# Kernel optimization log

Measured on AMD Instinct MI355X. Metric: run time of the kernel, lower is better.

The kernel has to match this reference:

```python
import jax, jax.numpy as jnp
import numpy as np

CROP = 48
THRESHOLD = 0.5
IOU_THRESHOLD = 0.5


def _conv(x, w, b):
    # x: [N,H,W,C], w: [kh,kw,Cin,Cout]
    y = jax.lax.conv_general_dilated(x, w, (1, 1), 'VALID',
                                     dimension_numbers=('NHWC', 'HWIO', 'NHWC'))
    return y + b


def _prelu(x, a):
    # a broadcasts over the channel-last axis
    return jnp.where(x >= 0, x, a * x)


def _maxpool(x, k, s, p):
    return jax.lax.reduce_window(x, -jnp.inf, jax.lax.max,
                                 (1, k, k, 1), (1, s, s, 1),
                                 ((0, 0), (p, p), (p, p), (0, 0)))


def _nms_keep(boxes, scores, valid, iou_thr):
    # fixed-shape greedy NMS (torchvision semantics: suppress iou > thr)
    N = boxes.shape[0]
    s = jnp.where(valid, scores, -jnp.inf)
    order = jnp.argsort(-s)
    b = boxes[order]
    x1, y1, x2, y2 = b[:, 0], b[:, 1], b[:, 2], b[:, 3]
    area = (x2 - x1) * (y2 - y1)
    xx1 = jnp.maximum(x1[:, None], x1[None, :])
    yy1 = jnp.maximum(y1[:, None], y1[None, :])
    xx2 = jnp.minimum(x2[:, None], x2[None, :])
    yy2 = jnp.minimum(y2[:, None], y2[None, :])
    inter = jnp.clip(xx2 - xx1, 0.0) * jnp.clip(yy2 - yy1, 0.0)
    iou = inter / (area[:, None] + area[None, :] - inter + 1e-12)
    keep0 = valid[order]
    idx = jnp.arange(N)

    def body(i, keep):
        sup = (iou[i] > iou_thr) & (idx > i) & keep[i] & keep
        return keep & ~sup

    keep_sorted = jax.lax.fori_loop(0, N, body, keep0)
    return jnp.zeros(N, bool).at[order].set(keep_sorted)


def setup_inputs() -> dict:
    key = jax.random.key(0)
    ks = jax.random.split(key, 24)
    H = W = 1024
    N = 2048
    image = jax.random.uniform(ks[0], (H, W, 3), jnp.float32) * 255.0
    x1 = jax.random.uniform(ks[1], (N,), jnp.float32) * (W - 130)
    y1 = jax.random.uniform(ks[2], (N,), jnp.float32) * (H - 130)
    bw = 20.0 + jax.random.uniform(ks[3], (N,), jnp.float32) * 100.0
    bh = 20.0 + jax.random.uniform(ks[4], (N,), jnp.float32) * 100.0
    bboxes = jnp.stack([x1, y1, x1 + bw, y1 + bh], axis=1)
    rn = lambda k, sh, s: jax.random.normal(k, sh, jnp.float32) * s
    return {
        'bboxes': bboxes, 'image': image,
        'conv1_w': rn(ks[5], (3, 3, 3, 32), 0.05), 'conv1_b': rn(ks[6], (32,), 0.01),
        'prelu1': 0.25 * jnp.ones((32,), jnp.float32),
        'conv2_w': rn(ks[7], (3, 3, 32, 64), 0.05), 'conv2_b': rn(ks[8], (64,), 0.01),
        'prelu2': 0.25 * jnp.ones((64,), jnp.float32),
        'conv3_w': rn(ks[9], (3, 3, 64, 64), 0.05), 'conv3_b': rn(ks[10], (64,), 0.01),
        'prelu3': 0.25 * jnp.ones((64,), jnp.float32),
        'conv4_w': rn(ks[11], (2, 2, 64, 128), 0.05), 'conv4_b': rn(ks[12], (128,), 0.01),
        'prelu4': 0.25 * jnp.ones((128,), jnp.float32),
        'fc5_w': rn(ks[13], (256, 1152), 0.02), 'fc5_b': rn(ks[14], (256,), 0.01),
        'prelu5': 0.25 * jnp.ones((256,), jnp.float32),
        'fc6a_w': rn(ks[15], (2, 256), 0.1), 'fc6a_b': rn(ks[16], (2,), 0.01),
        'fc6b_w': rn(ks[17], (4, 256), 0.1), 'fc6b_b': rn(ks[18], (4,), 0.01),
    }


def reference(bboxes, image, conv1_w, conv1_b, prelu1, conv2_w, conv2_b, prelu2,
              conv3_w, conv3_b, prelu3, conv4_w, conv4_b, prelu4,
              fc5_w, fc5_b, prelu5, fc6a_w, fc6a_b, fc6b_w, fc6b_b):
    H, W = image.shape[0], image.shape[1]
    N = bboxes.shape[0]
    # preprocess (torch: (x - 127.5) * 0.0078125)
    data = (image - 127.5) * 0.0078125  # [H,W,3]
    # clip boxes in place like the torch forward
    bx1 = jnp.clip(bboxes[:, 0], 0.0, None)
    by1 = jnp.clip(bboxes[:, 1], 0.0, None)
    bx2 = jnp.clip(bboxes[:, 2], None, float(W))
    by2 = jnp.clip(bboxes[:, 3], None, float(H))
    bb = jnp.stack([bx1, by1, bx2, by2], axis=1)  # clipped boxes [N,4]
    # integer crop windows (torch .int() truncation; coords >= 0)
    ib = bb.astype(jnp.int32)
    cw = jnp.maximum(ib[:, 2] - ib[:, 0], 1)
    ch = jnp.maximum(ib[:, 3] - ib[:, 1], 1)
    # nearest-neighbor resize to 48x48 (F.interpolate default mode='nearest')
    r = jnp.arange(CROP, dtype=jnp.int32)
    xs = ib[:, 0:1] + (r[None, :] * cw[:, None]) // CROP  # [N,48]
    ys = ib[:, 1:2] + (r[None, :] * ch[:, None]) // CROP  # [N,48]
    crops = data[ys[:, :, None], xs[:, None, :], :]  # [N,48,48,3] gather
    # CNN trunk
    h = _maxpool(_prelu(_conv(crops, conv1_w, conv1_b), prelu1), 3, 2, 1)
    h = _maxpool(_prelu(_conv(h, conv2_w, conv2_b), prelu2), 3, 2, 0)
    h = _maxpool(_prelu(_conv(h, conv3_w, conv3_b), prelu3), 2, 2, 0)
    h = _prelu(_conv(h, conv4_w, conv4_b), prelu4)  # [N,3,3,128]
    h = jnp.transpose(h, (0, 3, 1, 2)).reshape(N, -1)  # NCHW flatten like torch -> [N,1152]
    h = _prelu(h @ fc5_w.T + fc5_b, prelu5)  # [N,256]
    cls = jax.nn.softmax(h @ fc6a_w.T + fc6a_b, axis=1)  # [N,2]
    reg = h @ fc6b_w.T + fc6b_b  # [N,4]
    score = cls[:, 1]
    valid = score >= THRESHOLD
    w = bb[:, 2] - bb[:, 0]
    hgt = bb[:, 3] - bb[:, 1]
    out = jnp.stack([bb[:, 0] + reg[:, 0] * w,
                     bb[:, 1] + reg[:, 1] * hgt,
                     bb[:, 2] + reg[:, 2] * w,
                     bb[:, 3] + reg[:, 3] * hgt], axis=1)  # [N,4]
    keep = _nms_keep(out, score, valid, IOU_THRESHOLD)
    return jnp.where(keep[:, None], out, 0.0)
```

## Files before the change

kernel.cpp:

```cpp
#include <hip/hip_runtime.h>
#include <math.h>
#include <stdint.h>

#define NBOX 2048

__device__ __forceinline__ void fma4(float4& a, float s, const float4& w) {
  a.x = fmaf(s, w.x, a.x); a.y = fmaf(s, w.y, a.y);
  a.z = fmaf(s, w.z, a.z); a.w = fmaf(s, w.w, a.w);
}
__device__ __forceinline__ float4 max4(float4 a, float4 b) {
  return make_float4(fmaxf(a.x,b.x), fmaxf(a.y,b.y), fmaxf(a.z,b.z), fmaxf(a.w,b.w));
}
__device__ __forceinline__ float4 prelu4(float4 v, float4 a) {
  float4 r;
  r.x = v.x >= 0.f ? v.x : a.x*v.x;
  r.y = v.y >= 0.f ? v.y : a.y*v.y;
  r.z = v.z >= 0.f ? v.z : a.z*v.z;
  r.w = v.w >= 0.f ? v.w : a.w*v.w;
  return r;
}

__global__ __launch_bounds__(256) void k1_crop_conv1(
    const float* __restrict__ bboxes, const float* __restrict__ image,
    const float* __restrict__ w1, const float* __restrict__ b1, const float* __restrict__ a1,
    float* __restrict__ p1ws, int box0)
{
  __shared__ float crop[48*48*3];
  __shared__ float w1s[27*32];
  __shared__ float b1s[32], a1s[32];
  const int tid = threadIdx.x;
  const int n = box0 + blockIdx.x;

  for (int idx = tid; idx < 27*32; idx += 256) w1s[idx] = w1[idx];
  if (tid < 32) { b1s[tid] = b1[tid]; a1s[tid] = a1[tid]; }

  float f0 = bboxes[n*4+0], f1 = bboxes[n*4+1], f2 = bboxes[n*4+2], f3 = bboxes[n*4+3];
  float bx1 = fmaxf(f0, 0.f), by1 = fmaxf(f1, 0.f);
  float bx2 = fminf(f2, 1024.f), by2 = fminf(f3, 1024.f);
  int ix1 = (int)bx1, iy1 = (int)by1, ix2 = (int)bx2, iy2 = (int)by2;
  int cw = ix2 - ix1; if (cw < 1) cw = 1;
  int ch = iy2 - iy1; if (ch < 1) ch = 1;

  for (int idx = tid; idx < 6912; idx += 256) {
    int c = idx % 3; int t = idx / 3; int j = t % 48; int i = t / 48;
    int gx = ix1 + (j * cw) / 48;
    int gy = iy1 + (i * ch) / 48;
    float v = image[(gy*1024 + gx)*3 + c];
    crop[idx] = (v - 127.5f) * 0.0078125f;
  }
  __syncthreads();

  float* p1o = p1ws + (size_t)blockIdx.x * 17664;

  for (int slot = tid; slot < 1104; slot += 256) {
    int cq = slot & 7;
    int t2 = slot >> 3;
    int pjq = t2 % 6;
    int pi  = t2 / 6;
    int pj0 = pjq * 4;
    int c0 = 2*pj0 - 1;
    float4 bias  = *(const float4*)&b1s[cq*4];
    float4 alpha = *(const float4*)&a1s[cq*4];
    float4 mx[4];
#pragma unroll
    for (int t = 0; t < 4; t++) mx[t] = make_float4(-3.0e38f,-3.0e38f,-3.0e38f,-3.0e38f);

#pragma unroll
    for (int dr = 0; dr < 3; dr++) {
      int r = 2*pi - 1 + dr;
      if (r < 0 || r > 45) continue;
      float4 acc[9];
#pragma unroll
      for (int c = 0; c < 9; c++) acc[c] = bias;
#pragma unroll
      for (int kh = 0; kh < 3; kh++) {
        int row = r + kh;
        float s[33];
#pragma unroll
        for (int d = 0; d < 11; d++) {
          int cc = c0 + d; cc = cc < 0 ? 0 : (cc > 47 ? 47 : cc);
          int base = row*144 + cc*3;
          s[d*3+0] = crop[base+0];
          s[d*3+1] = crop[base+1];
          s[d*3+2] = crop[base+2];
        }
#pragma unroll
        for (int kw = 0; kw < 3; kw++) {
#pragma unroll
          for (int ci = 0; ci < 3; ci++) {
            float4 w = *(const float4*)&w1s[((kh*3+kw)*3+ci)*32 + cq*4];
#pragma unroll
            for (int c = 0; c < 9; c++) fma4(acc[c], s[(c+kw)*3+ci], w);
          }
        }
      }
#pragma unroll
      for (int c = 0; c < 9; c++) {
        int cabs = c0 + c;
        if (cabs < 0 || cabs > 45) continue;
        float4 pv = prelu4(acc[c], alpha);
#pragma unroll
        for (int t = 0; t < 4; t++) {
          if (c >= 2*t && c <= 2*t+2) mx[t] = max4(mx[t], pv);
        }
      }
    }
#pragma unroll
    for (int t = 0; t < 4; t++) {
      int pj = pj0 + t;
      if (pj < 23) {
        int base = pi*24 + pj;
        p1o[(cq*4+0)*552 + base] = mx[t].x;
        p1o[(cq*4+1)*552 + base] = mx[t].y;
        p1o[(cq*4+2)*552 + base] = mx[t].z;
        p1o[(cq*4+3)*552 + base] = mx[t].w;
      }
    }
  }
}

__global__ __launch_bounds__(128) void k2_conv2(
    const float* __restrict__ w2, const float* __restrict__ b2, const float* __restrict__ a2,
    const float* __restrict__ p1ws, float* __restrict__ p2ws)
{
  __shared__ float p1s[32*7*24];
  __shared__ float w2s[96*32];
  __shared__ float c2s[5*21*36];
  __shared__ float b2s[64], a2s[64];
  const int tid = threadIdx.x;
  const int bl = blockIdx.x / 5;
  const int pg = blockIdx.x % 5;
  const float* p1o = p1ws + (size_t)bl * 17664;
  float* p2o = p2ws + (size_t)bl * 7680;

  if (tid < 64) { b2s[tid] = b2[tid]; a2s[tid] = a2[tid]; }
  for (int idx4 = tid; idx4 < 1344; idx4 += 128) {
    int ci = idx4 / 42; int rr4 = idx4 % 42;
    *(float4*)&p1s[ci*168 + rr4*4] = *(const float4*)&p1o[ci*552 + pg*96 + rr4*4];
  }

  const int slot = tid;
  const bool active = slot < 120;
  const int cq = slot & 7, jt = (slot >> 3) % 3, rl = slot / 24;
  const int j0 = jt * 7;

  for (int half = 0; half < 2; half++) {
    float4 acc[7];
    for (int kh = 0; kh < 3; kh++) {
      __syncthreads();
      for (int idx4 = tid; idx4 < 768; idx4 += 128) {
        int col4 = idx4 & 7, kwci = idx4 >> 3;
        *(float4*)&w2s[kwci*32 + col4*4] =
            *(const float4*)&w2[(kh*96 + kwci)*64 + half*32 + col4*4];
      }
      __syncthreads();
      if (kh == 0) {
        float4 bias = *(const float4*)&b2s[half*32 + cq*4];
#pragma unroll
        for (int v = 0; v < 7; v++) acc[v] = bias;
      }
      if (active) {
        for (int ci = 0; ci < 32; ci++) {
          const float* ap = &p1s[ci*168 + (rl+kh)*24 + j0];
          float s[9];
#pragma unroll
          for (int d = 0; d < 9; d++) s[d] = ap[d];
#pragma unroll
          for (int kw = 0; kw < 3; kw++) {
            float4 w = *(const float4*)&w2s[(kw*32+ci)*32 + cq*4];
#pragma unroll
            for (int v = 0; v < 7; v++) fma4(acc[v], s[v+kw], w);
          }
        }
      }
    }
    if (active) {
      float4 alpha = *(const float4*)&a2s[half*32 + cq*4];
#pragma unroll
      for (int v = 0; v < 7; v++) {
        float4 p = prelu4(acc[v], alpha);
        *(float4*)&c2s[(rl*21 + j0+v)*36 + cq*4] = p;
      }
    }
    __syncthreads();
    for (int s2 = tid; s2 < 160; s2 += 128) {
      int pcq = s2 & 7, pj = (s2 >> 3) % 10, pp = s2 / 80;
      float4 m = make_float4(-3.0e38f,-3.0e38f,-3.0e38f,-3.0e38f);
#pragma unroll
      for (int dr = 0; dr < 3; dr++)
#pragma unroll
        for (int dc = 0; dc < 3; dc++)
          m = max4(m, *(const float4*)&c2s[((2*pp+dr)*21 + 2*pj+dc)*36 + pcq*4]);
      int pi = 2*pg + pp;
      int co = half*32 + pcq*4;
      p2o[(co+0)*120 + pi*12 + pj] = m.x;
      p2o[(co+1)*120 + pi*12 + pj] = m.y;
      p2o[(co+2)*120 + pi*12 + pj] = m.z;
      p2o[(co+3)*120 + pi*12 + pj] = m.w;
    }
    __syncthreads();
  }
}

__global__ __launch_bounds__(256) void k3_conv3(
    const float* __restrict__ w3, const float* __restrict__ b3, const float* __restrict__ a3,
    const float* __restrict__ p2ws, float* __restrict__ p3ws)
{
  __shared__ float p2s[7680];
  __shared__ float w3s[48*64];
  __shared__ float c3s[64*68];
  __shared__ float b3s[64], a3s[64];
  const int tid = threadIdx.x;
  const float* p2o = p2ws + (size_t)blockIdx.x * 7680;
  float* p3o = p3ws + (size_t)blockIdx.x * 1024;
  if (tid < 64) { b3s[tid] = b3[tid]; a3s[tid] = a3[tid]; }
  for (int idx4 = tid; idx4 < 1920; idx4 += 256)
    *(float4*)&p2s[idx4*4] = *(const float4*)&p2o[idx4*4];

  const int cq = tid & 15, jt = (tid >> 4) & 1, rl = tid >> 5;
  const int j0 = jt*4;
  float4 acc[4];
  bool first = true;

  for (int kh = 0; kh < 3; kh++) {
    for (int cg = 0; cg < 4; cg++) {
      __syncthreads();
      for (int idx4 = tid; idx4 < 768; idx4 += 256) {
        int co4 = idx4 & 15, kwcl = idx4 >> 4;
        int kw = kwcl >> 4, cl = kwcl & 15;
        *(float4*)&w3s[kwcl*64 + co4*4] =
            *(const float4*)&w3[((kh*3+kw)*64 + cg*16 + cl)*64 + co4*4];
      }
      __syncthreads();
      if (first) {
        float4 b = *(const float4*)&b3s[cq*4];
        acc[0]=b; acc[1]=b; acc[2]=b; acc[3]=b; first=false;
      }
      for (int cl = 0; cl < 16; cl++) {
        const float* ap = &p2s[(cg*16+cl)*120 + (rl+kh)*12 + j0];
        float s[6];
#pragma unroll
        for (int d = 0; d < 6; d++) s[d] = ap[d];
#pragma unroll
        for (int kw = 0; kw < 3; kw++) {
          float4 w = *(const float4*)&w3s[(kw*16+cl)*64 + cq*4];
#pragma unroll
          for (int v = 0; v < 4; v++) fma4(acc[v], s[v+kw], w);
        }
      }
    }
  }
  float4 alpha = *(const float4*)&a3s[cq*4];
#pragma unroll
  for (int v = 0; v < 4; v++) {
    float4 p = prelu4(acc[v], alpha);
    *(float4*)&c3s[(rl*8 + j0+v)*68 + cq*4] = p;
  }
  __syncthreads();
  {
    int pcq = tid & 15, pj = (tid >> 4) & 3, pi = tid >> 6;
    float4 m = make_float4(-3.0e38f,-3.0e38f,-3.0e38f,-3.0e38f);
#pragma unroll
    for (int dr = 0; dr < 2; dr++)
#pragma unroll
      for (int dc = 0; dc < 2; dc++)
        m = max4(m, *(const float4*)&c3s[((2*pi+dr)*8 + 2*pj+dc)*68 + pcq*4]);
    p3o[(pcq*4+0)*16 + pi*4 + pj] = m.x;
    p3o[(pcq*4+1)*16 + pi*4 + pj] = m.y;
    p3o[(pcq*4+2)*16 + pi*4 + pj] = m.z;
    p3o[(pcq*4+3)*16 + pi*4 + pj] = m.w;
  }
}

__global__ __launch_bounds__(128) void k4_conv4(
    const float* __restrict__ w4, const float* __restrict__ b4, const float* __restrict__ a4,
    const float* __restrict__ p3ws, float* __restrict__ c4ws)
{
  __shared__ float p3s[1024];
  __shared__ float w4s[64*128];
  __shared__ float b4s[128], a4s[128];
  const int tid = threadIdx.x;
  const float* p3o = p3ws + (size_t)blockIdx.x * 1024;
  float* c4o = c4ws + (size_t)blockIdx.x * 1152;
  b4s[tid] = b4[tid]; a4s[tid] = a4[tid];
  for (int idx4 = tid; idx4 < 256; idx4 += 128)
    *(float4*)&p3s[idx4*4] = *(const float4*)&p3o[idx4*4];

  const int slot = tid;
  const bool active = slot < 96;
  const int cq = slot & 31, rl = slot >> 5;
  float4 acc[3];
  bool first = true;
  for (int cg = 0; cg < 4; cg++) {
    __syncthreads();
    for (int idx4 = tid; idx4 < 2048; idx4 += 128) {
      int co4 = idx4 & 31, kkcl = idx4 >> 5;
      int khkw = kkcl >> 4, cl = kkcl & 15;
      *(float4*)&w4s[kkcl*128 + co4*4] =
          *(const float4*)&w4[(khkw*64 + cg*16 + cl)*128 + co4*4];
    }
    __syncthreads();
    if (active) {
      if (first) {
        float4 b = *(const float4*)&b4s[cq*4];
        acc[0]=b; acc[1]=b; acc[2]=b; first=false;
      }
      for (int cl = 0; cl < 16; cl++) {
        int ci = cg*16 + cl;
#pragma unroll
        for (int kh = 0; kh < 2; kh++) {
          float4 sv = *(const float4*)&p3s[ci*16 + (rl+kh)*4];
          float s[4] = {sv.x, sv.y, sv.z, sv.w};
#pragma unroll
          for (int kw = 0; kw < 2; kw++) {
            float4 w = *(const float4*)&w4s[((kh*2+kw)*16+cl)*128 + cq*4];
#pragma unroll
            for (int v = 0; v < 3; v++) fma4(acc[v], s[v+kw], w);
          }
        }
      }
    }
  }
  if (active) {
    float4 alpha = *(const float4*)&a4s[cq*4];
#pragma unroll
    for (int v = 0; v < 3; v++) {
      float4 p = prelu4(acc[v], alpha);
      c4o[(cq*4+0)*9 + rl*3 + v] = p.x;
      c4o[(cq*4+1)*9 + rl*3 + v] = p.y;
      c4o[(cq*4+2)*9 + rl*3 + v] = p.z;
      c4o[(cq*4+3)*9 + rl*3 + v] = p.w;
    }
  }
}

__global__ __launch_bounds__(256) void k5_fc(
    const float* __restrict__ fc5w, const float* __restrict__ fc5b, const float* __restrict__ a5,
    const float* __restrict__ w6a, const float* __restrict__ b6a,
    const float* __restrict__ w6b, const float* __restrict__ b6b,
    const float* __restrict__ bboxes, const float* __restrict__ c4ws,
    float* __restrict__ ws_scores, float* __restrict__ ws_boxes, int box0)
{
  __shared__ float c4s[8*1152];
  __shared__ float hs[8*256];
  __shared__ float l6[8][6];
  __shared__ float b5s[256], a5s[256];
  const int tid = threadIdx.x;
  const int lb0 = blockIdx.x * 8;
  b5s[tid] = fc5b[tid]; a5s[tid] = a5[tid];
  for (int idx4 = tid; idx4 < 2304; idx4 += 256)
    *(float4*)&c4s[idx4*4] = *(const float4*)&c4ws[(size_t)lb0*1152 + idx4*4];
  __syncthreads();

  const int og = tid & 31, bl = tid >> 5;
  float acc[8] = {0,0,0,0,0,0,0,0};
  const float* cbase = &c4s[bl*1152];
  for (int k = 0; k < 1152; k += 4) {
    float4 a = *(const float4*)&cbase[k];
#pragma unroll
    for (int u = 0; u < 8; u++) {
      int o = og + 32*u;
      float4 w = *(const float4*)&fc5w[(size_t)o*1152 + k];
      acc[u] += a.x*w.x + a.y*w.y + a.z*w.z + a.w*w.w;
    }
  }
#pragma unroll
  for (int u = 0; u < 8; u++) {
    int o = og + 32*u;
    float h = acc[u] + b5s[o];
    h = h >= 0.f ? h : a5s[o]*h;
    hs[bl*256 + o] = h;
  }
  __syncthreads();
  if (tid < 48) {
    int b = tid / 6, oi = tid % 6;
    const float* w = (oi < 2) ? &w6a[oi*256] : &w6b[(oi-2)*256];
    float d = (oi < 2) ? b6a[oi] : b6b[oi-2];
    const float* hh = &hs[b*256];
    for (int k = 0; k < 256; k++) d += hh[k]*w[k];
    l6[b][oi] = d;
  }
  __syncthreads();
  if (tid < 8) {
    int n = box0 + lb0 + tid;
    float l0 = l6[tid][0], l1 = l6[tid][1];
    float m = fmaxf(l0, l1);
    float e0 = expf(l0-m), e1 = expf(l1-m);
    float score = e1/(e0+e1);
    float r0 = l6[tid][2], r1 = l6[tid][3], r2 = l6[tid][4], r3 = l6[tid][5];
    float f0 = bboxes[n*4+0], f1 = bboxes[n*4+1], f2 = bboxes[n*4+2], f3 = bboxes[n*4+3];
    float bx1 = fmaxf(f0, 0.f), by1 = fmaxf(f1, 0.f);
    float bx2 = fminf(f2, 1024.f), by2 = fminf(f3, 1024.f);
    float w_ = bx2-bx1, h_ = by2-by1;
    ws_scores[n] = score;
    float4 ob = make_float4(bx1 + r0*w_, by1 + r1*h_, bx2 + r2*w_, by2 + r3*h_);
    *(float4*)&ws_boxes[n*4] = ob;
  }
}

__global__ __launch_bounds__(1024) void k6a_sort(
    const float* __restrict__ ws_scores, const float* __restrict__ ws_boxes,
    int* __restrict__ sidx_ws, float* __restrict__ sbox_ws,
    float* __restrict__ area_ws, int* __restrict__ nv_ws)
{
  __shared__ float skey[2048];
  __shared__ int   sidx[2048];
  const int tid = threadIdx.x;
  for (int i = tid; i < 2048; i += 1024) {
    float s = ws_scores[i];
    skey[i] = (s >= 0.5f) ? s : -INFINITY;
    sidx[i] = i;
  }
  __syncthreads();
  for (int k = 2; k <= 2048; k <<= 1) {
    for (int j = k >> 1; j > 0; j >>= 1) {
      for (int i = tid; i < 2048; i += 1024) {
        int ixj = i ^ j;
        if (ixj > i) {
          float a = skey[i], b = skey[ixj];
          int ia = sidx[i], ib = sidx[ixj];
          bool up = ((i & k) == 0);
          bool aAfterB = (a < b) || (a == b && ia > ib);
          if (up ? aAfterB : !aAfterB) {
            skey[i] = b; skey[ixj] = a; sidx[i] = ib; sidx[ixj] = ia;
          }
        }
      }
      __syncthreads();
    }
  }
  if (tid == 0) nv_ws[0] = 2048;
  __syncthreads();
  for (int i = tid; i < 2048; i += 1024) {
    if (skey[i] == -INFINITY && (i == 0 || skey[i-1] != -INFINITY)) nv_ws[0] = i;
    int n = sidx[i];
    sidx_ws[i] = n;
    float4 b = *(const float4*)&ws_boxes[n*4];
    *(float4*)&sbox_ws[i*4] = b;
    area_ws[i] = (b.z-b.x)*(b.w-b.y);
  }
}

__global__ __launch_bounds__(256) void k6b_iou(
    const int* __restrict__ nv_ws, const float* __restrict__ sbox_ws,
    const float* __restrict__ area_ws, unsigned long long* __restrict__ M)
{
  const int nv = nv_ws[0];
  int gt = blockIdx.x*256 + threadIdx.x;
  for (int w = gt; w < 2048*32; w += 128*256) {
    int i = w >> 5, wg = w & 31;
    if (i >= nv) continue;
    float4 bi = *(const float4*)&sbox_ws[i*4];
    float ai = area_ws[i];
    unsigned long long m = 0;
    int jbase = wg*64;
    if (jbase + 63 > i) {
      for (int jj = 0; jj < 64; jj++) {
        int j = jbase + jj;
        if (j <= i) continue;
        float4 bj = *(const float4*)&sbox_ws[j*4];
        float xx1 = fmaxf(bi.x, bj.x), yy1 = fmaxf(bi.y, bj.y);
        float xx2 = fminf(bi.z, bj.z), yy2 = fminf(bi.w, bj.w);
        float iw = fmaxf(xx2-xx1, 0.f), ih = fmaxf(yy2-yy1, 0.f);
        float inter = iw*ih;
        float iou = inter / (ai + area_ws[j] - inter + 1e-12f);
        if (iou > 0.5f) m |= (1ull << jj);
      }
    }
    M[w] = m;
  }
}

__global__ __launch_bounds__(1024) void k6c_scan(
    const int* __restrict__ nv_ws, const int* __restrict__ sidx_ws,
    const float* __restrict__ sbox_ws, const unsigned long long* __restrict__ M,
    float* __restrict__ out)
{
  __shared__ unsigned long long Msh[128*32];
  __shared__ unsigned long long rem_sh[32];
  const int tid = threadIdx.x;
  const int nv = nv_ws[0];
  unsigned long long rem = 0;

  for (int c0 = 0; c0 < 2048; c0 += 128) {
    if (c0 >= nv) break;
    for (int w = tid; w < 128*32; w += 1024) {
      int i = c0 + (w >> 5);
      if (i < nv) Msh[w] = M[(size_t)i*32 + (w & 31)];
    }
    __syncthreads();
    if (tid < 64) {
      int iend = c0 + 128; if (iend > nv) iend = nv;
      for (int i = c0; i < iend; i += 4) {
        unsigned long long m0=0, m1=0, m2=0, m3=0;
        int base = (i - c0) << 5;
        if (tid < 32) {
          m0 = Msh[base + tid];
          if (i+1 < iend) m1 = Msh[base + 32 + tid];
          if (i+2 < iend) m2 = Msh[base + 64 + tid];
          if (i+3 < iend) m3 = Msh[base + 96 + tid];
        }
        unsigned long long rw = __shfl(rem, (i >> 6), 64);
        if (!((rw >> (i & 63)) & 1ull)) rem |= m0;
        if (i+1 < iend) {
          rw = __shfl(rem, ((i+1) >> 6), 64);
          if (!((rw >> ((i+1) & 63)) & 1ull)) rem |= m1;
        }
        if (i+2 < iend) {
          rw = __shfl(rem, ((i+2) >> 6), 64);
          if (!((rw >> ((i+2) & 63)) & 1ull)) rem |= m2;
        }
        if (i+3 < iend) {
          rw = __shfl(rem, ((i+3) >> 6), 64);
          if (!((rw >> ((i+3) & 63)) & 1ull)) rem |= m3;
        }
      }
    }
    __syncthreads();
  }
  if (tid < 32) rem_sh[tid] = rem;
  __syncthreads();
  for (int i = tid; i < 2048; i += 1024) {
    bool keep = (i < nv) && !((rem_sh[i >> 6] >> (i & 63)) & 1ull);
    int n = sidx_ws[i];
    float4 b = *(const float4*)&sbox_ws[i*4];
    float4 o = keep ? b : make_float4(0.f,0.f,0.f,0.f);
    *(float4*)&out[n*4] = o;
  }
}

extern "C" void kernel_launch(void* const* d_in, const int* in_sizes, int n_in,
                              void* d_out, int out_size, void* d_ws, size_t ws_size,
                              hipStream_t stream)
{
  const float* bboxes = (const float*)d_in[0];
  const float* image  = (const float*)d_in[1];
  const float* w1 = (const float*)d_in[2];  const float* b1 = (const float*)d_in[3];  const float* a1 = (const float*)d_in[4];
  const float* w2 = (const float*)d_in[5];  const float* b2 = (const float*)d_in[6];  const float* a2 = (const float*)d_in[7];
  const float* w3 = (const float*)d_in[8];  const float* b3 = (const float*)d_in[9];  const float* a3 = (const float*)d_in[10];
  const float* w4 = (const float*)d_in[11]; const float* b4 = (const float*)d_in[12]; const float* a4 = (const float*)d_in[13];
  const float* fc5w = (const float*)d_in[14]; const float* fc5b = (const float*)d_in[15]; const float* a5 = (const float*)d_in[16];
  const float* w6a = (const float*)d_in[17]; const float* b6a = (const float*)d_in[18];
  const float* w6b = (const float*)d_in[19]; const float* b6b = (const float*)d_in[20];
  float* out = (float*)d_out;

  char* ws = (char*)d_ws;
  size_t off = 0;
  auto alloc = [&](size_t bytes) -> size_t {
    size_t p = off; off += (bytes + 255) & ~(size_t)255; return p;
  };
  size_t o_scores = alloc(NBOX*4);
  size_t o_boxes  = alloc(NBOX*16);
  size_t o_sidx   = alloc(NBOX*4);
  size_t o_sbox   = alloc(NBOX*16);
  size_t o_area   = alloc(NBOX*4);
  size_t o_nv     = alloc(256);
  size_t o_M      = alloc((size_t)NBOX*32*8);
  size_t fixed = off;
  const size_t perbox = (size_t)(17664 + 7680 + 1024 + 1152) * 4;

  int B = NBOX;
  if (fixed + (size_t)B*perbox > ws_size) {
    size_t avail = ws_size > fixed ? ws_size - fixed : 0;
    B = (int)(avail / perbox);
    B &= ~7;
    if (B < 8) B = 8;
    if (B > NBOX) B = NBOX;
  }
  size_t o_p1 = alloc((size_t)B*17664*4);
  size_t o_p2 = alloc((size_t)B*7680*4);
  size_t o_p3 = alloc((size_t)B*1024*4);
  size_t o_c4 = alloc((size_t)B*1152*4);

  float* ws_scores = (float*)(ws + o_scores);
  float* ws_boxes  = (float*)(ws + o_boxes);
  int*   sidxp     = (int*)(ws + o_sidx);
  float* sboxp     = (float*)(ws + o_sbox);
  float* areap     = (float*)(ws + o_area);
  int*   nvp       = (int*)(ws + o_nv);
  unsigned long long* Mp = (unsigned long long*)(ws + o_M);
  float* p1p = (float*)(ws + o_p1);
  float* p2p = (float*)(ws + o_p2);
  float* p3p = (float*)(ws + o_p3);
  float* c4p = (float*)(ws + o_c4);

  for (int c0 = 0; c0 < NBOX; c0 += B) {
    int Bc = NBOX - c0; if (Bc > B) Bc = B;
    k1_crop_conv1<<<Bc, 256, 0, stream>>>(bboxes, image, w1, b1, a1, p1p, c0);
    k2_conv2<<<Bc*5, 128, 0, stream>>>(w2, b2, a2, p1p, p2p);
    k3_conv3<<<Bc, 256, 0, stream>>>(w3, b3, a3, p2p, p3p);
    k4_conv4<<<Bc, 128, 0, stream>>>(w4, b4, a4, p3p, c4p);
    k5_fc<<<Bc/8, 256, 0, stream>>>(fc5w, fc5b, a5, w6a, b6a, w6b, b6b,
                                    bboxes, c4p, ws_scores, ws_boxes, c0);
  }
  k6a_sort<<<1, 1024, 0, stream>>>(ws_scores, ws_boxes, sidxp, sboxp, areap, nvp);
  k6b_iou<<<128, 256, 0, stream>>>(nvp, sboxp, areap, Mp);
  k6c_scan<<<1, 1024, 0, stream>>>(nvp, sidxp, sboxp, Mp, out);
}
```

Before: 1.718 ms.

## Restructure conv2/conv3 to wave-per-channel-group with register weights and shuffle pooling

The conv2 and conv3 kernels are rewritten so each 64-lane wave owns 8 output channels and computes over the whole spatial map. Weights are loaded straight from global memory into registers with double buffering, replacing the shared-memory weight staging and its repeated block barriers. Max-pooling is done through cross-lane shuffles instead of a shared-memory round trip. conv3 now processes two boxes per block. The cost is heavier register pressure and some idle lanes.

```diff
diff --git a/kernel.cpp b/kernel.cpp
--- a/kernel.cpp
+++ b/kernel.cpp
@@ -10,6 +10,9 @@
 }
 __device__ __forceinline__ float4 max4(float4 a, float4 b) {
   return make_float4(fmaxf(a.x,b.x), fmaxf(a.y,b.y), fmaxf(a.z,b.z), fmaxf(a.w,b.w));
+}
+__device__ __forceinline__ float4 max34(float4 a, float4 b, float4 c) {
+  return max4(max4(a, b), c);
 }
 __device__ __forceinline__ float4 prelu4(float4 v, float4 a) {
   float4 r;
@@ -17,6 +20,12 @@
   r.y = v.y >= 0.f ? v.y : a.y*v.y;
   r.z = v.z >= 0.f ? v.z : a.z*v.z;
   r.w = v.w >= 0.f ? v.w : a.w*v.w;
+  return r;
+}
+__device__ __forceinline__ float4 shfl4(float4 v, int src) {
+  float4 r;
+  r.x = __shfl(v.x, src, 64); r.y = __shfl(v.y, src, 64);
+  r.z = __shfl(v.z, src, 64); r.w = __shfl(v.w, src, 64);
   return r;
 }
 
@@ -119,156 +128,202 @@
   }
 }
 
-__global__ __launch_bounds__(128) void k2_conv2(
+#define K2_LOADW(W, CI, KH) { \
+  const float* wp_ = w2 + (((KH)*3)*32 + (CI))*64 + co0; \
+  W[0] = *(const float4*)(wp_);            W[1] = *(const float4*)(wp_ + 4); \
+  W[2] = *(const float4*)(wp_ + 2048);     W[3] = *(const float4*)(wp_ + 2052); \
+  W[4] = *(const float4*)(wp_ + 4096);     W[5] = *(const float4*)(wp_ + 4100); }
+
+#define K2_COMP(W, CI, KH) { \
+  const float* ip_ = &in_s[(CI)*552 + (rl+(KH))*24 + j0]; \
+  float s_[9]; \
+  _Pragma("unroll") for (int d_ = 0; d_ < 9; d_++) s_[d_] = ip_[d_]; \
+  _Pragma("unroll") for (int kw_ = 0; kw_ < 3; kw_++) { \
+    _Pragma("unroll") for (int jj_ = 0; jj_ < 7; jj_++) { \
+      fma4(acc[jj_][0], s_[jj_+kw_], W[kw_*2]); \
+      fma4(acc[jj_][1], s_[jj_+kw_], W[kw_*2+1]); } } }
+
+#define K2_STORE8(PJ, LO, HI) { \
+  float* d_ = p2o + (size_t)co0*120 + pi*12 + (PJ); \
+  float4 lo_ = (LO), hi_ = (HI); \
+  d_[0]   = lo_.x; d_[120] = lo_.y; d_[240] = lo_.z; d_[360] = lo_.w; \
+  d_[480] = hi_.x; d_[600] = hi_.y; d_[720] = hi_.z; d_[840] = hi_.w; }
+
+__global__ __launch_bounds__(512, 4) void k2_conv2(
     const float* __restrict__ w2, const float* __restrict__ b2, const float* __restrict__ a2,
     const float* __restrict__ p1ws, float* __restrict__ p2ws)
 {
-  __shared__ float p1s[32*7*24];
-  __shared__ float w2s[96*32];
-  __shared__ float c2s[5*21*36];
-  __shared__ float b2s[64], a2s[64];
+  __shared__ float in_s[17664];
   const int tid = threadIdx.x;
-  const int bl = blockIdx.x / 5;
-  const int pg = blockIdx.x % 5;
-  const float* p1o = p1ws + (size_t)bl * 17664;
-  float* p2o = p2ws + (size_t)bl * 7680;
-
-  if (tid < 64) { b2s[tid] = b2[tid]; a2s[tid] = a2[tid]; }
-  for (int idx4 = tid; idx4 < 1344; idx4 += 128) {
-    int ci = idx4 / 42; int rr4 = idx4 % 42;
-    *(float4*)&p1s[ci*168 + rr4*4] = *(const float4*)&p1o[ci*552 + pg*96 + rr4*4];
-  }
-
-  const int slot = tid;
-  const bool active = slot < 120;
-  const int cq = slot & 7, jt = (slot >> 3) % 3, rl = slot / 24;
+  const float* p1o = p1ws + (size_t)blockIdx.x * 17664;
+  float* p2o = p2ws + (size_t)blockIdx.x * 7680;
+
+  for (int i4 = tid; i4 < 4416; i4 += 512)
+    *(float4*)&in_s[i4*4] = *(const float4*)&p1o[i4*4];
+  __syncthreads();
+
+  const int wav = __builtin_amdgcn_readfirstlane(tid >> 6);
+  const int lane = tid & 63;
+  int jt = lane / 21;
+  int rl = lane - jt * 21;
+  if (lane == 63) { jt = 2; rl = 20; }
   const int j0 = jt * 7;
-
-  for (int half = 0; half < 2; half++) {
-    float4 acc[7];
-    for (int kh = 0; kh < 3; kh++) {
-      __syncthreads();
-      for (int idx4 = tid; idx4 < 768; idx4 += 128) {
-        int col4 = idx4 & 7, kwci = idx4 >> 3;
-        *(float4*)&w2s[kwci*32 + col4*4] =
-            *(const float4*)&w2[(kh*96 + kwci)*64 + half*32 + col4*4];
-      }
-      __syncthreads();
-      if (kh == 0) {
-        float4 bias = *(const float4*)&b2s[half*32 + cq*4];
-#pragma unroll
-        for (int v = 0; v < 7; v++) acc[v] = bias;
-      }
-      if (active) {
-        for (int ci = 0; ci < 32; ci++) {
-          const float* ap = &p1s[ci*168 + (rl+kh)*24 + j0];
-          float s[9];
-#pragma unroll
-          for (int d = 0; d < 9; d++) s[d] = ap[d];
-#pragma unroll
-          for (int kw = 0; kw < 3; kw++) {
-            float4 w = *(const float4*)&w2s[(kw*32+ci)*32 + cq*4];
-#pragma unroll
-            for (int v = 0; v < 7; v++) fma4(acc[v], s[v+kw], w);
-          }
-        }
-      }
-    }
-    if (active) {
-      float4 alpha = *(const float4*)&a2s[half*32 + cq*4];
-#pragma unroll
-      for (int v = 0; v < 7; v++) {
-        float4 p = prelu4(acc[v], alpha);
-        *(float4*)&c2s[(rl*21 + j0+v)*36 + cq*4] = p;
-      }
-    }
-    __syncthreads();
-    for (int s2 = tid; s2 < 160; s2 += 128) {
-      int pcq = s2 & 7, pj = (s2 >> 3) % 10, pp = s2 / 80;
-      float4 m = make_float4(-3.0e38f,-3.0e38f,-3.0e38f,-3.0e38f);
-#pragma unroll
-      for (int dr = 0; dr < 3; dr++)
-#pragma unroll
-        for (int dc = 0; dc < 3; dc++)
-          m = max4(m, *(const float4*)&c2s[((2*pp+dr)*21 + 2*pj+dc)*36 + pcq*4]);
-      int pi = 2*pg + pp;
-      int co = half*32 + pcq*4;
-      p2o[(co+0)*120 + pi*12 + pj] = m.x;
-      p2o[(co+1)*120 + pi*12 + pj] = m.y;
-      p2o[(co+2)*120 + pi*12 + pj] = m.z;
-      p2o[(co+3)*120 + pi*12 + pj] = m.w;
-    }
-    __syncthreads();
-  }
-}
-
-__global__ __launch_bounds__(256) void k3_conv3(
+  const int co0 = wav * 8;
+
+  float4 bL = *(const float4*)&b2[co0];
+  float4 bH = *(const float4*)&b2[co0+4];
+  float4 aL = *(const float4*)&a2[co0];
+  float4 aH = *(const float4*)&a2[co0+4];
+
+  float4 acc[7][2];
+#pragma unroll
+  for (int jj = 0; jj < 7; jj++) { acc[jj][0] = bL; acc[jj][1] = bH; }
+
+  float4 wA[6], wB[6];
+  K2_LOADW(wA, 0, 0);
+#pragma unroll 1
+  for (int ci = 0; ci < 32; ci += 2) {
+    K2_LOADW(wB, ci, 1);
+    K2_COMP(wA, ci, 0);
+    K2_LOADW(wA, ci, 2);
+    K2_COMP(wB, ci, 1);
+    K2_LOADW(wB, ci+1, 0);
+    K2_COMP(wA, ci, 2);
+    K2_LOADW(wA, ci+1, 1);
+    K2_COMP(wB, ci+1, 0);
+    K2_LOADW(wB, ci+1, 2);
+    K2_COMP(wA, ci+1, 1);
+    if (ci + 2 < 32) K2_LOADW(wA, ci+2, 0);
+    K2_COMP(wB, ci+1, 2);
+  }
+
+#pragma unroll
+  for (int jj = 0; jj < 7; jj++) {
+    acc[jj][0] = prelu4(acc[jj][0], aL);
+    acc[jj][1] = prelu4(acc[jj][1], aH);
+  }
+
+#pragma unroll
+  for (int jj = 0; jj < 7; jj++) {
+#pragma unroll
+    for (int h = 0; h < 2; h++) {
+      float4 v = acc[jj][h];
+      float4 d1 = shfl4(v, lane + 1);
+      float4 d2 = shfl4(v, lane + 2);
+      acc[jj][h] = max34(v, d1, d2);
+    }
+  }
+  float4 r0[2], r1[2];
+#pragma unroll
+  for (int h = 0; h < 2; h++) {
+    r0[h] = shfl4(acc[0][h], lane + 21);
+    r1[h] = shfl4(acc[1][h], lane + 21);
+  }
+
+  if (((rl & 1) == 0) && rl <= 18) {
+    const int pi = rl >> 1;
+    if (jt == 0) {
+      K2_STORE8(0, max34(acc[0][0],acc[1][0],acc[2][0]), max34(acc[0][1],acc[1][1],acc[2][1]));
+      K2_STORE8(1, max34(acc[2][0],acc[3][0],acc[4][0]), max34(acc[2][1],acc[3][1],acc[4][1]));
+      K2_STORE8(2, max34(acc[4][0],acc[5][0],acc[6][0]), max34(acc[4][1],acc[5][1],acc[6][1]));
+      K2_STORE8(3, max34(acc[6][0],r0[0],r1[0]),          max34(acc[6][1],r0[1],r1[1]));
+    } else if (jt == 1) {
+      K2_STORE8(4, max34(acc[1][0],acc[2][0],acc[3][0]), max34(acc[1][1],acc[2][1],acc[3][1]));
+      K2_STORE8(5, max34(acc[3][0],acc[4][0],acc[5][0]), max34(acc[3][1],acc[4][1],acc[5][1]));
+      K2_STORE8(6, max34(acc[5][0],acc[6][0],r0[0]),     max34(acc[5][1],acc[6][1],r0[1]));
+    } else {
+      K2_STORE8(7, max34(acc[0][0],acc[1][0],acc[2][0]), max34(acc[0][1],acc[1][1],acc[2][1]));
+      K2_STORE8(8, max34(acc[2][0],acc[3][0],acc[4][0]), max34(acc[2][1],acc[3][1],acc[4][1]));
+      K2_STORE8(9, max34(acc[4][0],acc[5][0],acc[6][0]), max34(acc[4][1],acc[5][1],acc[6][1]));
+    }
+  }
+}
+
+#define K3_LOADW(W, CI, KH) { \
+  const float* wp_ = w3 + (((KH)*3)*64 + (CI))*64 + co0; \
+  W[0] = *(const float4*)(wp_);            W[1] = *(const float4*)(wp_ + 4); \
+  W[2] = *(const float4*)(wp_ + 4096);     W[3] = *(const float4*)(wp_ + 4100); \
+  W[4] = *(const float4*)(wp_ + 8192);     W[5] = *(const float4*)(wp_ + 8196); }
+
+#define K3_COMP(W, CI, KH) { \
+  const float* ip_ = ibase + (CI)*120 + (KH)*12; \
+  float2 sA_ = *(const float2*)(ip_); \
+  float2 sB_ = *(const float2*)(ip_ + 2); \
+  float s_[4] = {sA_.x, sA_.y, sB_.x, sB_.y}; \
+  _Pragma("unroll") for (int kw_ = 0; kw_ < 3; kw_++) { \
+    _Pragma("unroll") for (int c_ = 0; c_ < 2; c_++) { \
+      fma4(acc[c_][0], s_[c_+kw_], W[kw_*2]); \
+      fma4(acc[c_][1], s_[c_+kw_], W[kw_*2+1]); } } }
+
+__global__ __launch_bounds__(512, 4) void k3_conv3(
     const float* __restrict__ w3, const float* __restrict__ b3, const float* __restrict__ a3,
     const float* __restrict__ p2ws, float* __restrict__ p3ws)
 {
-  __shared__ float p2s[7680];
-  __shared__ float w3s[48*64];
-  __shared__ float c3s[64*68];
-  __shared__ float b3s[64], a3s[64];
+  __shared__ float in_s[15376];
   const int tid = threadIdx.x;
-  const float* p2o = p2ws + (size_t)blockIdx.x * 7680;
-  float* p3o = p3ws + (size_t)blockIdx.x * 1024;
-  if (tid < 64) { b3s[tid] = b3[tid]; a3s[tid] = a3[tid]; }
-  for (int idx4 = tid; idx4 < 1920; idx4 += 256)
-    *(float4*)&p2s[idx4*4] = *(const float4*)&p2o[idx4*4];
-
-  const int cq = tid & 15, jt = (tid >> 4) & 1, rl = tid >> 5;
-  const int j0 = jt*4;
-  float4 acc[4];
-  bool first = true;
-
-  for (int kh = 0; kh < 3; kh++) {
-    for (int cg = 0; cg < 4; cg++) {
-      __syncthreads();
-      for (int idx4 = tid; idx4 < 768; idx4 += 256) {
-        int co4 = idx4 & 15, kwcl = idx4 >> 4;
-        int kw = kwcl >> 4, cl = kwcl & 15;
-        *(float4*)&w3s[kwcl*64 + co4*4] =
-            *(const float4*)&w3[((kh*3+kw)*64 + cg*16 + cl)*64 + co4*4];
-      }
-      __syncthreads();
-      if (first) {
-        float4 b = *(const float4*)&b3s[cq*4];
-        acc[0]=b; acc[1]=b; acc[2]=b; acc[3]=b; first=false;
-      }
-      for (int cl = 0; cl < 16; cl++) {
-        const float* ap = &p2s[(cg*16+cl)*120 + (rl+kh)*12 + j0];
-        float s[6];
-#pragma unroll
-        for (int d = 0; d < 6; d++) s[d] = ap[d];
-#pragma unroll
-        for (int kw = 0; kw < 3; kw++) {
-          float4 w = *(const float4*)&w3s[(kw*16+cl)*64 + cq*4];
-#pragma unroll
-          for (int v = 0; v < 4; v++) fma4(acc[v], s[v+kw], w);
-        }
-      }
-    }
-  }
-  float4 alpha = *(const float4*)&a3s[cq*4];
-#pragma unroll
-  for (int v = 0; v < 4; v++) {
-    float4 p = prelu4(acc[v], alpha);
-    *(float4*)&c3s[(rl*8 + j0+v)*68 + cq*4] = p;
-  }
-  __syncthreads();
-  {
-    int pcq = tid & 15, pj = (tid >> 4) & 3, pi = tid >> 6;
-    float4 m = make_float4(-3.0e38f,-3.0e38f,-3.0e38f,-3.0e38f);
-#pragma unroll
-    for (int dr = 0; dr < 2; dr++)
-#pragma unroll
-      for (int dc = 0; dc < 2; dc++)
-        m = max4(m, *(const float4*)&c3s[((2*pi+dr)*8 + 2*pj+dc)*68 + pcq*4]);
-    p3o[(pcq*4+0)*16 + pi*4 + pj] = m.x;
-    p3o[(pcq*4+1)*16 + pi*4 + pj] = m.y;
-    p3o[(pcq*4+2)*16 + pi*4 + pj] = m.z;
-    p3o[(pcq*4+3)*16 + pi*4 + pj] = m.w;
+  const float* p2o = p2ws + (size_t)(blockIdx.x*2) * 7680;
+  float* p3o0 = p3ws + (size_t)(blockIdx.x*2) * 1024;
+
+  for (int i4 = tid; i4 < 3840; i4 += 512) {
+    int bb = (i4 >= 1920) ? 1 : 0;
+    int k = i4 - bb*1920;
+    *(float4*)&in_s[bb*7688 + k*4] = *(const float4*)&p2o[(size_t)bb*7680 + k*4];
+  }
+  __syncthreads();
+
+  const int wav = __builtin_amdgcn_readfirstlane(tid >> 6);
+  const int lane = tid & 63;
+  const int b  = lane >> 5;
+  const int r  = (lane >> 2) & 7;
+  const int cg = lane & 3;
+  const int co0 = wav * 8;
+
+  float4 bL = *(const float4*)&b3[co0];
+  float4 bH = *(const float4*)&b3[co0+4];
+  float4 aL = *(const float4*)&a3[co0];
+  float4 aH = *(const float4*)&a3[co0+4];
+
+  float4 acc[2][2];
+  acc[0][0] = bL; acc[0][1] = bH; acc[1][0] = bL; acc[1][1] = bH;
+
+  const float* ibase = &in_s[b*7688 + r*12 + cg*2];
+
+  float4 wA[6], wB[6];
+  K3_LOADW(wA, 0, 0);
+#pragma unroll 1
+  for (int ci = 0; ci < 64; ci += 2) {
+    K3_LOADW(wB, ci, 1);
+    K3_COMP(wA, ci, 0);
+    K3_LOADW(wA, ci, 2);
+    K3_COMP(wB, ci, 1);
+    K3_LOADW(wB, ci+1, 0);
+    K3_COMP(wA, ci, 2);
+    K3_LOADW(wA, ci+1, 1);
+    K3_COMP(wB, ci+1, 0);
+    K3_LOADW(wB, ci+1, 2);
+    K3_COMP(wA, ci+1, 1);
+    if (ci + 2 < 64) K3_LOADW(wA, ci+2, 0);
+    K3_COMP(wB, ci+1, 2);
+  }
+
+  float4 hm[2];
+#pragma unroll
+  for (int h = 0; h < 2; h++) {
+    float4 p0 = prelu4(acc[0][h], h ? aH : aL);
+    float4 p1 = prelu4(acc[1][h], h ? aH : aL);
+    hm[h] = max4(p0, p1);
+  }
+  float4 o[2];
+#pragma unroll
+  for (int h = 0; h < 2; h++) {
+    float4 d = shfl4(hm[h], lane + 4);
+    o[h] = max4(hm[h], d);
+  }
+  if ((r & 1) == 0) {
+    const int pi = r >> 1;
+    float* d = p3o0 + b*1024 + (size_t)co0*16 + pi*4 + cg;
+    d[0]   = o[0].x; d[16]  = o[0].y; d[32]  = o[0].z; d[48]  = o[0].w;
+    d[64]  = o[1].x; d[80]  = o[1].y; d[96]  = o[1].z; d[112] = o[1].w;
   }
 }
 
@@ -587,8 +642,8 @@
   for (int c0 = 0; c0 < NBOX; c0 += B) {
     int Bc = NBOX - c0; if (Bc > B) Bc = B;
     k1_crop_conv1<<<Bc, 256, 0, stream>>>(bboxes, image, w1, b1, a1, p1p, c0);
-    k2_conv2<<<Bc*5, 128, 0, stream>>>(w2, b2, a2, p1p, p2p);
-    k3_conv3<<<Bc, 256, 0, stream>>>(w3, b3, a3, p2p, p3p);
+    k2_conv2<<<Bc, 512, 0, stream>>>(w2, b2, a2, p1p, p2p);
+    k3_conv3<<<Bc/2, 512, 0, stream>>>(w3, b3, a3, p2p, p3p);
     k4_conv4<<<Bc, 128, 0, stream>>>(w4, b4, a4, p3p, c4p);
     k5_fc<<<Bc/8, 256, 0, stream>>>(fc5w, fc5b, a5, w6a, b6a, w6b, b6b,
                                     bboxes, c4p, ws_scores, ws_boxes, c0);
```

Measured after the change: 1.709 ms. Within noise of the previous version (-0.5%).
